# Kernel optimization log

Measured on AMD Instinct MI355X. Metric: run time of the kernel, lower is better.

## Reference

```python
import jax, jax.numpy as jnp
import numpy as np

H, C = 8, 32          # heads, channels per head; H*C = 256 triggers the LN branch
N_NODES = 30000       # nodes per node type
N_EDGES = 100000      # edges per edge type
N_TYPES = 6           # hardwired edge types (all src = Package_Name)
D_IN = 128            # raw input feature dim (Package_Name stays at 128)
LRELU_SLOPE = 0.2     # PyG GATConv default negative_slope


def _segment_softmax(e, dst, n):
    # softmax of per-edge logits e [E,H] grouped by destination node
    m = jax.ops.segment_max(e, dst, num_segments=n)
    ex = jnp.exp(e - m[dst])
    den = jax.ops.segment_sum(ex, dst, num_segments=n)
    return ex / (den[dst] + 1e-16)


def _gat(x_src, x_tgt, src, dst, Ws, Wd, a_s, a_d, b):
    # bipartite GATConv, concat heads, no self loops, no edge features
    hs = (x_src @ Ws).reshape(-1, H, C)   # [Ns,H,C]
    hd = (x_tgt @ Wd).reshape(-1, H, C)   # [Nt,H,C]
    es = jnp.einsum('nhc,hc->nh', hs, a_s)
    ed = jnp.einsum('nhc,hc->nh', hd, a_d)
    e = jax.nn.leaky_relu(es[src] + ed[dst], negative_slope=LRELU_SLOPE)  # [E,H]
    n = x_tgt.shape[0]
    alpha = _segment_softmax(e, dst, n)                                   # [E,H]
    msg = hs[src] * alpha[:, :, None]                                     # [E,H,C]
    out = jax.ops.segment_sum(msg, dst, num_segments=n).reshape(n, H * C) + b
    return out, alpha


def _ln_relu(x, g, b):
    mu = x.mean(-1, keepdims=True)
    var = ((x - mu) ** 2).mean(-1, keepdims=True)
    return jax.nn.relu((x - mu) / jnp.sqrt(var + 1e-5) * g + b)


def setup_inputs() -> dict:
    key = jax.random.key(0)
    ks = jax.random.split(key, 16)
    s = 0.05
    return {
        'x_pkg': jax.random.normal(ks[0], (N_NODES, D_IN), jnp.float32),
        'x_tgt': jax.random.normal(ks[1], (N_TYPES, N_NODES, D_IN), jnp.float32),
        'edge_index': jax.random.randint(ks[2], (N_TYPES, 2, N_EDGES), 0, N_NODES, jnp.int32),
        'W1_src': jax.random.normal(ks[3], (N_TYPES, D_IN, H * C), jnp.float32) * s,
        'W1_dst': jax.random.normal(ks[4], (N_TYPES, D_IN, H * C), jnp.float32) * s,
        'att1_src': jax.random.normal(ks[5], (N_TYPES, H, C), jnp.float32) * s,
        'att1_dst': jax.random.normal(ks[6], (N_TYPES, H, C), jnp.float32) * s,
        'b1': jnp.zeros((N_TYPES, H * C), jnp.float32),
        'W2_src': jax.random.normal(ks[7], (N_TYPES, D_IN, H * C), jnp.float32) * s,
        'W2_dst': jax.random.normal(ks[8], (N_TYPES, H * C, H * C), jnp.float32) * s,
        'att2_src': jax.random.normal(ks[9], (N_TYPES, H, C), jnp.float32) * s,
        'att2_dst': jax.random.normal(ks[10], (N_TYPES, H, C), jnp.float32) * s,
        'b2': jnp.zeros((N_TYPES, H * C), jnp.float32),
        'gamma': jnp.ones((N_TYPES, H * C), jnp.float32),
        'beta': jnp.zeros((N_TYPES, H * C), jnp.float32),
        'Wc': jax.random.normal(ks[11], (N_TYPES * H * C + D_IN, 1), jnp.float32) * s,
        'bc': jnp.zeros((1,), jnp.float32),
    }


def reference(x_pkg, x_tgt, edge_index, W1_src, W1_dst, att1_src, att1_dst, b1,
              W2_src, W2_dst, att2_src, att2_dst, b2, gamma, beta, Wc, bc):
    def layer(xt, ei, Ws, Wd, a_s, a_d, bb):
        return _gat(x_pkg, xt, ei[0], ei[1], Ws, Wd, a_s, a_d, bb)

    vlayer = jax.vmap(layer, in_axes=(0, 0, 0, 0, 0, 0, 0))

    # layer 1: Package_Name -> each of 6 target types; Package_Name itself unchanged
    out1, _ = vlayer(x_tgt, edge_index, W1_src, W1_dst, att1_src, att1_dst, b1)
    x1 = jax.vmap(_ln_relu)(out1, gamma, beta)   # module reuses ln1 after both layers

    # layer 2: src features are still the raw 128-d Package_Name features
    out2, alpha2 = vlayer(x1, edge_index, W2_src, W2_dst, att2_src, att2_dst, b2)
    x2 = jax.vmap(_ln_relu)(out2, gamma, beta)

    # global mean pool per node type, concat (6 targets then Package_Name), classify
    pooled = jnp.concatenate([x2.mean(axis=1).reshape(-1), x_pkg.mean(axis=0)])
    logits = pooled @ Wc[:, 0] + bc[0]
    return logits, alpha2
```

## Files before the change

kernel.cpp:

```cpp
#include <hip/hip_runtime.h>
#include <hip/hip_bf16.h>
#include <cstddef>

#define N_NODES 30000
#define N_EDGES 100000
#define N_TYPES 6
#define D_IN 128
#define HC 256
#define NH 8
#define CH 32

typedef __attribute__((ext_vector_type(8))) unsigned short ushort8_t;
typedef __attribute__((ext_vector_type(4))) unsigned short ushort4_t;
typedef __attribute__((ext_vector_type(8))) __bf16 bf16x8;
typedef __attribute__((ext_vector_type(4))) float floatx4;

#define L2_NPB 16
#define L2_GRID ((N_NODES + L2_NPB - 1) / L2_NPB)

__device__ inline unsigned short f2bf(float f) {
    unsigned u = __float_as_uint(f);
    u += 0x7fffu + ((u >> 16) & 1u);
    return (unsigned short)(u >> 16);
}
__device__ inline float bf2f(unsigned short u) {
    return __uint_as_float(((unsigned)u) << 16);
}

__global__ void zero4(float4* __restrict__ p, int n4) {
    int g = blockIdx.x * blockDim.x + threadIdx.x;
    if (g < n4) p[g] = make_float4(0.f, 0.f, 0.f, 0.f);
}
__global__ void zero_i(int* __restrict__ p, int n) {
    int g = blockIdx.x * blockDim.x + threadIdx.x;
    if (g < n) p[g] = 0;
}
__global__ void to_bf16(const float* __restrict__ x, unsigned short* __restrict__ o, int n4) {
    int g = blockIdx.x * blockDim.x + threadIdx.x;
    if (g >= n4) return;
    float4 v = ((const float4*)x)[g];
    ushort4_t p;
    p[0] = f2bf(v.x); p[1] = f2bf(v.y); p[2] = f2bf(v.z); p[3] = f2bf(v.w);
    *(ushort4_t*)&o[(size_t)g * 4] = p;
}

__global__ void hist_all(const int* __restrict__ ei, int* __restrict__ counts) {
    int t = blockIdx.y;
    int e = blockIdx.x * 256 + threadIdx.x;
    if (e < N_EDGES)
        atomicAdd(&counts[t * N_NODES + ei[(size_t)t * 2 * N_EDGES + N_EDGES + e]], 1);
}

#define SCAN_T 1024
#define SCAN_C 30
__global__ __launch_bounds__(1024) void scan_all(const int* __restrict__ counts_g,
                                                 int* __restrict__ row_ptr_g,
                                                 int* __restrict__ cursor_g) {
    int t = blockIdx.x;
    const int* counts = counts_g + t * N_NODES;
    int* row_ptr = row_ptr_g + t * (N_NODES + 1);
    int* cursor = cursor_g + t * N_NODES;
    __shared__ int part[SCAN_T];
    int tid = threadIdx.x;
    int base = tid * SCAN_C;
    int loc[SCAN_C];
    int s = 0;
    #pragma unroll
    for (int i = 0; i < SCAN_C; ++i) {
        int idx = base + i;
        int v = (idx < N_NODES) ? counts[idx] : 0;
        loc[i] = s; s += v;
    }
    part[tid] = s;
    __syncthreads();
    int tot = s;
    for (int d = 1; d < SCAN_T; d <<= 1) {
        int v = (tid >= d) ? part[tid - d] : 0;
        __syncthreads();
        part[tid] += v;
        __syncthreads();
    }
    int off = part[tid] - tot;
    #pragma unroll
    for (int i = 0; i < SCAN_C; ++i) {
        int idx = base + i;
        if (idx < N_NODES) { int r = off + loc[i]; row_ptr[idx] = r; cursor[idx] = r; }
    }
    if (tid == SCAN_T - 1) row_ptr[N_NODES] = part[SCAN_T - 1];
}

__global__ void fill_all(const int* __restrict__ ei, int* __restrict__ cursor,
                         int* __restrict__ elist) {
    int t = blockIdx.y;
    int e = blockIdx.x * 256 + threadIdx.x;
    if (e < N_EDGES) {
        const int* src = ei + (size_t)t * 2 * N_EDGES;
        const int* dst = src + N_EDGES;
        int pos = atomicAdd(&cursor[t * N_NODES + dst[e]], 1);
        elist[t * N_EDGES + pos] = src[e];
    }
}

__global__ void att_weight_all(const float* __restrict__ W1d, const float* __restrict__ a1d,
                               const float* __restrict__ W2d, const float* __restrict__ a2d,
                               float* __restrict__ wd1, float* __restrict__ wd2) {
    int g = blockIdx.x * blockDim.x + threadIdx.x;
    const int per_t = (D_IN + HC) * NH;
    if (g >= N_TYPES * per_t) return;
    int t = g / per_t, r = g % per_t;
    if (r < D_IN * NH) {
        int k = r >> 3, h = r & 7;
        const float* wr = W1d + (size_t)t * D_IN * HC + (size_t)k * HC + h * CH;
        const float* ar = a1d + t * HC + h * CH;
        float s = 0.f;
        #pragma unroll
        for (int c = 0; c < CH; ++c) s += wr[c] * ar[c];
        wd1[t * D_IN * NH + h * D_IN + k] = s;
    } else {
        r -= D_IN * NH;
        int k = r >> 3, h = r & 7;
        const float* wr = W2d + (size_t)t * HC * HC + (size_t)k * HC + h * CH;
        const float* ar = a2d + t * HC + h * CH;
        float s = 0.f;
        #pragma unroll
        for (int c = 0; c < CH; ++c) s += wr[c] * ar[c];
        wd2[t * HC * NH + h * HC + k] = s;
    }
}

__global__ __launch_bounds__(256) void ed1_all(const float* __restrict__ x_tgt,
                                               const float* __restrict__ wd1,
                                               float* __restrict__ ed1g) {
    const int t = blockIdx.y;
    const int lane = threadIdx.x & 63;
    const int wv = threadIdx.x >> 6;
    const int n8 = lane >> 3, h = lane & 7;
    const int node = blockIdx.x * 32 + wv * 8 + n8;
    if (node >= N_NODES) return;
    const float* xr = x_tgt + ((size_t)t * N_NODES + node) * D_IN;
    const float* wp = wd1 + t * D_IN * NH + h * D_IN;
    float acc = 0.f;
    #pragma unroll
    for (int k = 0; k < D_IN; k += 4) {
        const float4 x4 = *(const float4*)&xr[k];
        const float4 w4 = *(const float4*)&wp[k];
        acc += x4.x * w4.x + x4.y * w4.y + x4.z * w4.z + x4.w * w4.w;
    }
    ed1g[((size_t)t * N_NODES + node) * NH + h] = acc;
}

__global__ __launch_bounds__(256) void gemm_all(const unsigned short* __restrict__ A,
                                                const float* __restrict__ W1s,
                                                const float* __restrict__ W2s,
                                                const float* __restrict__ att1,
                                                const float* __restrict__ att2,
                                                unsigned short* __restrict__ hs_all,
                                                float* __restrict__ es_all) {
    const int j = blockIdx.z;
    const float* B = (j < 6) ? W1s + (size_t)j * D_IN * HC
                             : W2s + (size_t)(j - 6) * D_IN * HC;
    const float* att = (j < 6) ? att1 + j * HC : att2 + (j - 6) * HC;
    unsigned short* Cp = hs_all + (size_t)j * N_NODES * HC;
    float* e_out = es_all + (size_t)j * N_NODES * NH;

    __shared__ unsigned short As[64 * 40];
    __shared__ unsigned short Bs[64 * 40];

    const int tid = threadIdx.x;
    const int w = tid >> 6;
    const int lane = tid & 63;
    const int col = lane & 15;
    const int quad = lane >> 4;
    const int m0 = blockIdx.x * 64;
    const int n0 = blockIdx.y * 64;

    const int am = tid >> 2;
    const int ak = (tid & 3) * 8;
    const int bk2 = (tid >> 4) * 2;
    const int bn4 = (tid & 15) * 4;

    floatx4 acc[4];
    #pragma unroll
    for (int ct = 0; ct < 4; ++ct) acc[ct] = (floatx4){0.f, 0.f, 0.f, 0.f};

    #pragma unroll
    for (int k0 = 0; k0 < D_IN; k0 += 32) {
        {
            int gm = m0 + am;
            ushort8_t v = (ushort8_t){0, 0, 0, 0, 0, 0, 0, 0};
            if (gm < N_NODES) v = *(const ushort8_t*)&A[(size_t)gm * D_IN + k0 + ak];
            *(ushort8_t*)&As[am * 40 + ak] = v;
        }
        {
            const float4 r0 = *(const float4*)&B[(size_t)(k0 + bk2) * HC + n0 + bn4];
            const float4 r1 = *(const float4*)&B[(size_t)(k0 + bk2 + 1) * HC + n0 + bn4];
            float a0[4] = {r0.x, r0.y, r0.z, r0.w};
            float a1[4] = {r1.x, r1.y, r1.z, r1.w};
            #pragma unroll
            for (int q = 0; q < 4; ++q) {
                unsigned pk = (unsigned)f2bf(a0[q]) | ((unsigned)f2bf(a1[q]) << 16);
                *(unsigned*)&Bs[(bn4 + q) * 40 + bk2] = pk;
            }
        }
        __syncthreads();
        {
            ushort8_t araw = *(const ushort8_t*)&As[(w * 16 + col) * 40 + quad * 8];
            bf16x8 af = __builtin_bit_cast(bf16x8, araw);
            #pragma unroll
            for (int ct = 0; ct < 4; ++ct) {
                ushort8_t braw = *(const ushort8_t*)&Bs[(ct * 16 + col) * 40 + quad * 8];
                bf16x8 bf = __builtin_bit_cast(bf16x8, braw);
                acc[ct] = __builtin_amdgcn_mfma_f32_16x16x32_bf16(af, bf, acc[ct], 0, 0, 0);
            }
        }
        __syncthreads();
    }

    #pragma unroll
    for (int ct = 0; ct < 4; ++ct) {
        #pragma unroll
        for (int r = 0; r < 4; ++r) {
            int gm = m0 + w * 16 + quad * 4 + r;
            if (gm < N_NODES) Cp[(size_t)gm * HC + n0 + ct * 16 + col] = f2bf(acc[ct][r]);
        }
    }

    float attv[4];
    #pragma unroll
    for (int ct = 0; ct < 4; ++ct) attv[ct] = att[n0 + ct * 16 + col];
    const int hbase = n0 >> 5;
    #pragma unroll
    for (int r = 0; r < 4; ++r) {
        float h0v = acc[0][r] * attv[0] + acc[1][r] * attv[1];
        float h1v = acc[2][r] * attv[2] + acc[3][r] * attv[3];
        #pragma unroll
        for (int off = 1; off < 16; off <<= 1) {
            h0v += __shfl_xor(h0v, off);
            h1v += __shfl_xor(h1v, off);
        }
        if (col == 0) {
            int gm = m0 + w * 16 + quad * 4 + r;
            if (gm < N_NODES) {
                e_out[gm * NH + hbase] = h0v;
                e_out[gm * NH + hbase + 1] = h1v;
            }
        }
    }
}

__device__ inline void edge4(const float* __restrict__ es,
                             const unsigned short* __restrict__ hs,
                             int s_pre, int i, int cm,
                             int h_l, int lane, float ed_mine,
                             float& den, float4& acc) {
    const int i1 = (i + 1 < cm) ? i + 1 : cm;
    const int i2 = (i + 2 < cm) ? i + 2 : cm;
    const int i3 = (i + 3 < cm) ? i + 3 : cm;
    const int s0 = __shfl(s_pre, i);
    const int s1 = __shfl(s_pre, i1);
    const int s2 = __shfl(s_pre, i2);
    const int s3 = __shfl(s_pre, i3);
    float q0 = es[s0 * NH + h_l];
    float q1 = es[s1 * NH + h_l];
    float q2 = es[s2 * NH + h_l];
    float q3 = es[s3 * NH + h_l];
    const ushort4_t v0 = *(const ushort4_t*)&hs[(size_t)s0 * HC + lane * 4];
    const ushort4_t v1 = *(const ushort4_t*)&hs[(size_t)s1 * HC + lane * 4];
    const ushort4_t v2 = *(const ushort4_t*)&hs[(size_t)s2 * HC + lane * 4];
    const ushort4_t v3 = *(const ushort4_t*)&hs[(size_t)s3 * HC + lane * 4];
    q0 += ed_mine; q0 = (q0 >= 0.f) ? q0 : 0.2f * q0;
    q1 += ed_mine; q1 = (q1 >= 0.f) ? q1 : 0.2f * q1;
    q2 += ed_mine; q2 = (q2 >= 0.f) ? q2 : 0.2f * q2;
    q3 += ed_mine; q3 = (q3 >= 0.f) ? q3 : 0.2f * q3;
    const float x0 = __expf(q0);
    const float x1 = (i + 1 <= cm) ? __expf(q1) : 0.f;
    const float x2 = (i + 2 <= cm) ? __expf(q2) : 0.f;
    const float x3 = (i + 3 <= cm) ? __expf(q3) : 0.f;
    den += (x0 + x1) + (x2 + x3);
    acc.x += x0 * bf2f(v0[0]) + x1 * bf2f(v1[0]) + x2 * bf2f(v2[0]) + x3 * bf2f(v3[0]);
    acc.y += x0 * bf2f(v0[1]) + x1 * bf2f(v1[1]) + x2 * bf2f(v2[1]) + x3 * bf2f(v3[1]);
    acc.z += x0 * bf2f(v0[2]) + x1 * bf2f(v1[2]) + x2 * bf2f(v2[2]) + x3 * bf2f(v3[2]);
    acc.w += x0 * bf2f(v0[3]) + x1 * bf2f(v1[3]) + x2 * bf2f(v2[3]) + x3 * bf2f(v3[3]);
}

__device__ inline void edge1(const float* __restrict__ es,
                             const unsigned short* __restrict__ hs,
                             int s, int h_l, int lane, float ed_mine,
                             float& den, float4& acc) {
    float x = es[s * NH + h_l] + ed_mine;
    x = (x >= 0.f) ? x : 0.2f * x;
    const float ex = __expf(x);
    den += ex;
    const ushort4_t hv = *(const ushort4_t*)&hs[(size_t)s * HC + lane * 4];
    acc.x += ex * bf2f(hv[0]); acc.y += ex * bf2f(hv[1]);
    acc.z += ex * bf2f(hv[2]); acc.w += ex * bf2f(hv[3]);
}

__global__ __launch_bounds__(256) void gather_l1_all(const int* __restrict__ row_ptr_g,
                                                     const int* __restrict__ elist_g,
                                                     const float* __restrict__ es_all,
                                                     const float* __restrict__ ed1g,
                                                     const unsigned short* __restrict__ hs_all,
                                                     const float* __restrict__ b1,
                                                     const float* __restrict__ gamma,
                                                     const float* __restrict__ beta,
                                                     const float* __restrict__ wd2,
                                                     float* __restrict__ ed2g_all) {
    const int t = blockIdx.y;
    const int* row_ptr = row_ptr_g + t * (N_NODES + 1);
    const int* elist = elist_g + t * N_EDGES;
    const float* es = es_all + (size_t)t * N_NODES * NH;
    const unsigned short* hs = hs_all + (size_t)t * N_NODES * HC;
    const float* bias = b1 + t * HC;
    const float* gam = gamma + t * HC;
    const float* bet = beta + t * HC;
    const float* w2 = wd2 + t * HC * NH;
    float* ed2g = ed2g_all + (size_t)t * N_NODES * NH;

    const int lane = threadIdx.x & 63;
    const int w = threadIdx.x >> 6;
    const int d = blockIdx.x * 4 + w;
    const int h_l = lane >> 3;

    const float ed_mine = ed1g[((size_t)t * N_NODES + d) * NH + h_l];
    const int e0 = row_ptr[d], e1n = row_ptr[d + 1];
    const int cnt = e1n - e0;
    int s_pre = 0;
    if (lane < cnt) s_pre = elist[e0 + lane];

    float den = 0.f;
    float4 acc = make_float4(0.f, 0.f, 0.f, 0.f);
    if (cnt > 0) {
        const int c1 = (cnt < 64) ? cnt : 64;
        const int cm = c1 - 1;
        for (int i = 0; i < c1; i += 4)
            edge4(es, hs, s_pre, i, cm, h_l, lane, ed_mine, den, acc);
        if (cnt > 64)
            for (int ii = e0 + 64; ii < e1n; ++ii)
                edge1(es, hs, elist[ii], h_l, lane, ed_mine, den, acc);
    }

    const float inv = 1.f / (den + 1e-16f);
    const float4 bv = *(const float4*)&bias[lane * 4];
    acc.x = acc.x * inv + bv.x; acc.y = acc.y * inv + bv.y;
    acc.z = acc.z * inv + bv.z; acc.w = acc.w * inv + bv.w;

    float s1 = acc.x + acc.y + acc.z + acc.w;
    float s2 = acc.x * acc.x + acc.y * acc.y + acc.z * acc.z + acc.w * acc.w;
    #pragma unroll
    for (int off = 1; off < 64; off <<= 1) { s1 += __shfl_xor(s1, off); s2 += __shfl_xor(s2, off); }
    const float mu = s1 * (1.f / 256.f);
    const float var = s2 * (1.f / 256.f) - mu * mu;
    const float rstd = rsqrtf(var + 1e-5f);
    const float4 g4 = *(const float4*)&gam[lane * 4];
    const float4 b4 = *(const float4*)&bet[lane * 4];
    const float ya0 = fmaxf((acc.x - mu) * rstd * g4.x + b4.x, 0.f);
    const float ya1 = fmaxf((acc.y - mu) * rstd * g4.y + b4.y, 0.f);
    const float ya2 = fmaxf((acc.z - mu) * rstd * g4.z + b4.z, 0.f);
    const float ya3 = fmaxf((acc.w - mu) * rstd * g4.w + b4.w, 0.f);

    __shared__ __align__(16) float ya_s[4][256];
    {
        const int c0 = lane * 4;
        const int widx = (c0 & ~31) | ((c0 & 31) ^ ((lane >> 3) << 2));
        *(float4*)&ya_s[w][widx] = make_float4(ya0, ya1, ya2, ya3);
    }
    const int k8 = lane >> 3;
    const int h = lane & 7;
    const float* w2h = w2 + h * HC;
    float e2 = 0.f;
    #pragma unroll
    for (int jj = 0; jj < 8; ++jj) {
        const int idx = k8 * 32 + ((jj * 4) ^ (k8 << 2));
        const float4 y = *(const float4*)&ya_s[w][idx];
        const float4 wv = *(const float4*)&w2h[k8 * 32 + jj * 4];
        e2 += y.x * wv.x + y.y * wv.y + y.z * wv.z + y.w * wv.w;
    }
    e2 += __shfl_xor(e2, 8);
    e2 += __shfl_xor(e2, 16);
    e2 += __shfl_xor(e2, 32);
    if (lane < 8) ed2g[d * NH + lane] = e2;
}

__global__ __launch_bounds__(256) void gather_l2_all(const int* __restrict__ row_ptr_g,
                                                     const int* __restrict__ elist_g,
                                                     const float* __restrict__ es_all,
                                                     const float* __restrict__ ed2g_all,
                                                     const unsigned short* __restrict__ hs_all,
                                                     const float* __restrict__ b2,
                                                     const float* __restrict__ gamma,
                                                     const float* __restrict__ beta,
                                                     float* __restrict__ deng_all,
                                                     float* __restrict__ ppart) {
    const int t = blockIdx.y;
    const int* row_ptr = row_ptr_g + t * (N_NODES + 1);
    const int* elist = elist_g + t * N_EDGES;
    const float* es = es_all + (size_t)(6 + t) * N_NODES * NH;
    const float* ed2g = ed2g_all + (size_t)t * N_NODES * NH;
    const unsigned short* hs = hs_all + (size_t)(6 + t) * N_NODES * HC;
    const float* bias = b2 + t * HC;
    const float* gam = gamma + t * HC;
    const float* bet = beta + t * HC;
    float* deng = deng_all + (size_t)t * N_NODES * NH;
    float* psum_part = ppart + (size_t)t * L2_GRID * HC;

    const int tid = threadIdx.x;
    const int lane = tid & 63;
    const int w = tid >> 6;
    const int h_l = lane >> 3;
    const float4 bv = *(const float4*)&bias[lane * 4];
    const float4 g4 = *(const float4*)&gam[lane * 4];
    const float4 b4 = *(const float4*)&bet[lane * 4];

    float4 pool = make_float4(0.f, 0.f, 0.f, 0.f);
    const int base = blockIdx.x * L2_NPB;

    #pragma unroll 1
    for (int rep = 0; rep < L2_NPB / 4; ++rep) {
        const int d = base + rep * 4 + w;
        if (d >= N_NODES) break;

        const float ed_mine = ed2g[d * NH + h_l];
        const int e0 = row_ptr[d], e1n = row_ptr[d + 1];
        const int cnt = e1n - e0;
        int s_pre = 0;
        if (lane < cnt) s_pre = elist[e0 + lane];

        float den = 0.f;
        float4 acc = make_float4(0.f, 0.f, 0.f, 0.f);
        if (cnt > 0) {
            const int c1 = (cnt < 64) ? cnt : 64;
            const int cm = c1 - 1;
            for (int i = 0; i < c1; i += 4)
                edge4(es, hs, s_pre, i, cm, h_l, lane, ed_mine, den, acc);
            if (cnt > 64)
                for (int ii = e0 + 64; ii < e1n; ++ii)
                    edge1(es, hs, elist[ii], h_l, lane, ed_mine, den, acc);
        }
        if ((lane & 7) == 0) deng[d * NH + h_l] = den;
        const float inv = 1.f / (den + 1e-16f);
        acc.x = acc.x * inv + bv.x; acc.y = acc.y * inv + bv.y;
        acc.z = acc.z * inv + bv.z; acc.w = acc.w * inv + bv.w;

        float s1 = acc.x + acc.y + acc.z + acc.w;
        float s2 = acc.x * acc.x + acc.y * acc.y + acc.z * acc.z + acc.w * acc.w;
        #pragma unroll
        for (int off = 1; off < 64; off <<= 1) { s1 += __shfl_xor(s1, off); s2 += __shfl_xor(s2, off); }
        const float mu = s1 * (1.f / 256.f);
        const float var = s2 * (1.f / 256.f) - mu * mu;
        const float rstd = rsqrtf(var + 1e-5f);
        pool.x += fmaxf((acc.x - mu) * rstd * g4.x + b4.x, 0.f);
        pool.y += fmaxf((acc.y - mu) * rstd * g4.y + b4.y, 0.f);
        pool.z += fmaxf((acc.z - mu) * rstd * g4.z + b4.z, 0.f);
        pool.w += fmaxf((acc.w - mu) * rstd * g4.w + b4.w, 0.f);
    }

    __shared__ __align__(16) float sacc[4][260];
    *(float4*)&sacc[w][lane * 4] = pool;
    __syncthreads();
    float tot = sacc[0][tid] + sacc[1][tid] + sacc[2][tid] + sacc[3][tid];
    psum_part[(size_t)blockIdx.x * HC + tid] = tot;
}

__global__ __launch_bounds__(256) void pool_reduce_all(const float* __restrict__ ppart,
                                                       float* __restrict__ psums) {
    int t = blockIdx.y;
    const float* part = ppart + (size_t)t * L2_GRID * HC;
    int tid = threadIdx.x;
    float acc = 0.f;
    for (int b = blockIdx.x; b < L2_GRID; b += gridDim.x)
        acc += part[(size_t)b * HC + tid];
    atomicAdd(&psums[t * HC + tid], acc);
}

__global__ void alpha_all(const int* __restrict__ ei,
                          const float* __restrict__ es_all,
                          const float* __restrict__ ed2g_all,
                          const float* __restrict__ deng_all,
                          float* __restrict__ out) {
    int t = blockIdx.y;
    int g = blockIdx.x * 256 + threadIdx.x;
    if (g >= N_EDGES * NH) return;
    int e = g >> 3, h = g & 7;
    const int* src = ei + (size_t)t * 2 * N_EDGES;
    const int* dst = src + N_EDGES;
    int s = src[e], d = dst[e];
    const float* es = es_all + (size_t)(6 + t) * N_NODES * NH;
    float x = es[s * NH + h] + ed2g_all[(size_t)t * N_NODES * NH + d * NH + h];
    x = (x >= 0.f) ? x : 0.2f * x;
    out[(size_t)t * N_EDGES * NH + g] =
        __expf(x) / (deng_all[(size_t)t * N_NODES * NH + d * NH + h] + 1e-16f);
}

__global__ __launch_bounds__(256) void pkg_accum(const float* __restrict__ x, float* __restrict__ sums) {
    int tid = threadIdx.x;
    int col = tid & 127;
    int rof = tid >> 7;
    float acc = 0.f;
    for (int r = blockIdx.x * 2 + rof; r < N_NODES; r += gridDim.x * 2)
        acc += x[(size_t)r * D_IN + col];
    atomicAdd(&sums[col], acc);
}

__global__ __launch_bounds__(256) void logits_k(const float* __restrict__ psums,
                                                const float* __restrict__ ksums,
                                                const float* __restrict__ Wc,
                                                const float* __restrict__ bc,
                                                float* __restrict__ out) {
    int tid = threadIdx.x;
    const float inv = 1.f / (float)N_NODES;
    float acc = 0.f;
    for (int i = tid; i < N_TYPES * HC; i += 256) acc += psums[i] * inv * Wc[i];
    if (tid < D_IN) acc += ksums[tid] * inv * Wc[N_TYPES * HC + tid];
    #pragma unroll
    for (int off = 32; off; off >>= 1) acc += __shfl_down(acc, off);
    __shared__ float w[4];
    if ((tid & 63) == 0) w[tid >> 6] = acc;
    __syncthreads();
    if (tid == 0) out[0] = w[0] + w[1] + w[2] + w[3] + bc[0];
}

static inline void zf(float* p, int n, hipStream_t stream) {
    int n4 = (n + 3) >> 2;
    zero4<<<(n4 + 255) / 256, 256, 0, stream>>>((float4*)p, n4);
}

extern "C" void kernel_launch(void* const* d_in, const int* in_sizes, int n_in,
                              void* d_out, int out_size, void* d_ws, size_t ws_size,
                              hipStream_t stream) {
    const float* x_pkg    = (const float*)d_in[0];
    const float* x_tgt    = (const float*)d_in[1];
    const int*   ei       = (const int*)d_in[2];
    const float* W1_src   = (const float*)d_in[3];
    const float* W1_dst   = (const float*)d_in[4];
    const float* att1_src = (const float*)d_in[5];
    const float* att1_dst = (const float*)d_in[6];
    const float* b1       = (const float*)d_in[7];
    const float* W2_src   = (const float*)d_in[8];
    const float* W2_dst   = (const float*)d_in[9];
    const float* att2_src = (const float*)d_in[10];
    const float* att2_dst = (const float*)d_in[11];
    const float* b2       = (const float*)d_in[12];
    const float* gamma    = (const float*)d_in[13];
    const float* beta     = (const float*)d_in[14];
    const float* Wc       = (const float*)d_in[15];
    const float* bc       = (const float*)d_in[16];
    float* out = (float*)d_out;

    char* wsb = (char*)d_ws;
    unsigned short* xpkg_bf = (unsigned short*)wsb;
    unsigned short* hs_all  = xpkg_bf + (size_t)N_NODES * D_IN;
    float* es_all   = (float*)(hs_all + (size_t)12 * N_NODES * HC);
    float* ed2g_all = es_all + (size_t)12 * N_NODES * NH;
    float* deng_all = ed2g_all + (size_t)N_TYPES * N_NODES * NH;
    float* psums    = deng_all + (size_t)N_TYPES * N_NODES * NH;
    float* ksums    = psums + N_TYPES * HC;
    float* wd1      = ksums + D_IN;
    float* wd2      = wd1 + N_TYPES * D_IN * NH;
    float* ed1g     = wd2 + N_TYPES * HC * NH;
    float* ppart    = ed1g + (size_t)N_TYPES * N_NODES * NH;
    int* counts  = (int*)(ppart + (size_t)N_TYPES * L2_GRID * HC);
    int* row_ptr = counts + N_TYPES * N_NODES;
    int* cursor  = row_ptr + N_TYPES * (N_NODES + 1);
    int* elist   = cursor + N_TYPES * N_NODES;

    dim3 egrid((N_EDGES + 255) / 256, N_TYPES);

    zf(psums, N_TYPES * HC, stream);
    zf(ksums, D_IN, stream);
    pkg_accum<<<256, 256, 0, stream>>>(x_pkg, ksums);
    {
        int tot = N_TYPES * (D_IN + HC) * NH;
        att_weight_all<<<(tot + 255) / 256, 256, 0, stream>>>(W1_dst, att1_dst, W2_dst, att2_dst, wd1, wd2);
    }
    {
        dim3 g((N_NODES + 31) / 32, N_TYPES);
        ed1_all<<<g, 256, 0, stream>>>(x_tgt, wd1, ed1g);
    }
    to_bf16<<<((N_NODES * D_IN / 4) + 255) / 256, 256, 0, stream>>>(x_pkg, xpkg_bf, N_NODES * D_IN / 4);
    zero_i<<<(N_TYPES * N_NODES + 255) / 256, 256, 0, stream>>>(counts, N_TYPES * N_NODES);
    hist_all<<<egrid, 256, 0, stream>>>(ei, counts);
    scan_all<<<N_TYPES, SCAN_T, 0, stream>>>(counts, row_ptr, cursor);
    fill_all<<<egrid, 256, 0, stream>>>(ei, cursor, elist);

    {
        dim3 g((N_NODES + 63) / 64, HC / 64, 12);
        gemm_all<<<g, 256, 0, stream>>>(xpkg_bf, W1_src, W2_src, att1_src, att2_src,
                                        hs_all, es_all);
    }

    {
        dim3 g(N_NODES / 4, N_TYPES);
        gather_l1_all<<<g, 256, 0, stream>>>(row_ptr, elist, es_all, ed1g, hs_all,
                                             b1, gamma, beta, wd2, ed2g_all);
    }

    {
        dim3 g(L2_GRID, N_TYPES);
        gather_l2_all<<<g, 256, 0, stream>>>(row_ptr, elist, es_all, ed2g_all, hs_all,
                                             b2, gamma, beta, deng_all, ppart);
    }
    {
        dim3 g(8, N_TYPES);
        pool_reduce_all<<<g, 256, 0, stream>>>(ppart, psums);
    }
    {
        dim3 g((N_EDGES * NH + 255) / 256, N_TYPES);
        alpha_all<<<g, 256, 0, stream>>>(ei, es_all, ed2g_all, deng_all, out + 1);
    }

    logits_k<<<1, 256, 0, stream>>>(psums, ksums, Wc, bc, out);
}
```

Measured before the change: 880.2 us.

## Fuse layer-1 and layer-2 gathers into one kernel with small-degree fast path

Layer 1 and layer 2 attention gathers now run in one kernel per destination node. The layer-2 logit term is kept in registers through a shuffle instead of being reloaded from global memory, and the second launch is removed. For nodes with at most four edges, the neighbour rows and logits for both layers are loaded together up front to hide latency. The trade-offs are a larger per-block pool partial buffer (one row per 4 nodes instead of per 16), more reduction work in pool_reduce (grid widened), and higher register pressure.

```diff
diff --git a/kernel.cpp b/kernel.cpp
--- a/kernel.cpp
+++ b/kernel.cpp
@@ -15,8 +15,7 @@
 typedef __attribute__((ext_vector_type(8))) __bf16 bf16x8;
 typedef __attribute__((ext_vector_type(4))) float floatx4;
 
-#define L2_NPB 16
-#define L2_GRID ((N_NODES + L2_NPB - 1) / L2_NPB)
+#define FG_GRID (N_NODES / 4)
 
 __device__ inline unsigned short f2bf(float f) {
     unsigned u = __float_as_uint(f);
@@ -296,26 +295,27 @@
     acc.z += ex * bf2f(hv[2]); acc.w += ex * bf2f(hv[3]);
 }
 
-__global__ __launch_bounds__(256) void gather_l1_all(const int* __restrict__ row_ptr_g,
-                                                     const int* __restrict__ elist_g,
-                                                     const float* __restrict__ es_all,
-                                                     const float* __restrict__ ed1g,
-                                                     const unsigned short* __restrict__ hs_all,
-                                                     const float* __restrict__ b1,
-                                                     const float* __restrict__ gamma,
-                                                     const float* __restrict__ beta,
-                                                     const float* __restrict__ wd2,
-                                                     float* __restrict__ ed2g_all) {
+__global__ __launch_bounds__(256) void fused_gather_all(
+        const int* __restrict__ row_ptr_g, const int* __restrict__ elist_g,
+        const float* __restrict__ es_all, const float* __restrict__ ed1g,
+        const unsigned short* __restrict__ hs_all,
+        const float* __restrict__ b1, const float* __restrict__ b2,
+        const float* __restrict__ gamma, const float* __restrict__ beta,
+        const float* __restrict__ wd2,
+        float* __restrict__ ed2g_all, float* __restrict__ deng_all,
+        float* __restrict__ ppart) {
     const int t = blockIdx.y;
     const int* row_ptr = row_ptr_g + t * (N_NODES + 1);
     const int* elist = elist_g + t * N_EDGES;
-    const float* es = es_all + (size_t)t * N_NODES * NH;
-    const unsigned short* hs = hs_all + (size_t)t * N_NODES * HC;
-    const float* bias = b1 + t * HC;
+    const float* es1 = es_all + (size_t)t * N_NODES * NH;
+    const float* es2 = es_all + (size_t)(6 + t) * N_NODES * NH;
+    const unsigned short* hs1 = hs_all + (size_t)t * N_NODES * HC;
+    const unsigned short* hs2 = hs_all + (size_t)(6 + t) * N_NODES * HC;
     const float* gam = gamma + t * HC;
     const float* bet = beta + t * HC;
     const float* w2 = wd2 + t * HC * NH;
     float* ed2g = ed2g_all + (size_t)t * N_NODES * NH;
+    float* deng = deng_all + (size_t)t * N_NODES * NH;
 
     const int lane = threadIdx.x & 63;
     const int w = threadIdx.x >> 6;
@@ -328,25 +328,66 @@
     int s_pre = 0;
     if (lane < cnt) s_pre = elist[e0 + lane];
 
-    float den = 0.f;
-    float4 acc = make_float4(0.f, 0.f, 0.f, 0.f);
-    if (cnt > 0) {
+    float den1 = 0.f, den2 = 0.f;
+    float4 acc1 = make_float4(0.f, 0.f, 0.f, 0.f);
+    float4 acc2 = make_float4(0.f, 0.f, 0.f, 0.f);
+
+    float q20, q21, q22, q23;
+    ushort4_t v20, v21, v22, v23;
+    const bool fast = (cnt > 0) && (cnt <= 4);
+
+    if (fast) {
+        const int cm = cnt - 1;
+        const int s0 = __shfl(s_pre, 0);
+        const int s1 = __shfl(s_pre, (1 < cm) ? 1 : cm);
+        const int s2 = __shfl(s_pre, (2 < cm) ? 2 : cm);
+        const int s3 = __shfl(s_pre, cm);
+        float q10 = es1[s0 * NH + h_l];
+        float q11 = es1[s1 * NH + h_l];
+        float q12 = es1[s2 * NH + h_l];
+        float q13 = es1[s3 * NH + h_l];
+        const ushort4_t v10 = *(const ushort4_t*)&hs1[(size_t)s0 * HC + lane * 4];
+        const ushort4_t v11 = *(const ushort4_t*)&hs1[(size_t)s1 * HC + lane * 4];
+        const ushort4_t v12 = *(const ushort4_t*)&hs1[(size_t)s2 * HC + lane * 4];
+        const ushort4_t v13 = *(const ushort4_t*)&hs1[(size_t)s3 * HC + lane * 4];
+        q20 = es2[s0 * NH + h_l];
+        q21 = es2[s1 * NH + h_l];
+        q22 = es2[s2 * NH + h_l];
+        q23 = es2[s3 * NH + h_l];
+        v20 = *(const ushort4_t*)&hs2[(size_t)s0 * HC + lane * 4];
+        v21 = *(const ushort4_t*)&hs2[(size_t)s1 * HC + lane * 4];
+        v22 = *(const ushort4_t*)&hs2[(size_t)s2 * HC + lane * 4];
+        v23 = *(const ushort4_t*)&hs2[(size_t)s3 * HC + lane * 4];
+        q10 += ed_mine; q10 = (q10 >= 0.f) ? q10 : 0.2f * q10;
+        q11 += ed_mine; q11 = (q11 >= 0.f) ? q11 : 0.2f * q11;
+        q12 += ed_mine; q12 = (q12 >= 0.f) ? q12 : 0.2f * q12;
+        q13 += ed_mine; q13 = (q13 >= 0.f) ? q13 : 0.2f * q13;
+        const float x0 = __expf(q10);
+        const float x1 = (cnt > 1) ? __expf(q11) : 0.f;
+        const float x2 = (cnt > 2) ? __expf(q12) : 0.f;
+        const float x3 = (cnt > 3) ? __expf(q13) : 0.f;
+        den1 = (x0 + x1) + (x2 + x3);
+        acc1.x = x0 * bf2f(v10[0]) + x1 * bf2f(v11[0]) + x2 * bf2f(v12[0]) + x3 * bf2f(v13[0]);
+        acc1.y = x0 * bf2f(v10[1]) + x1 * bf2f(v11[1]) + x2 * bf2f(v12[1]) + x3 * bf2f(v13[1]);
+        acc1.z = x0 * bf2f(v10[2]) + x1 * bf2f(v11[2]) + x2 * bf2f(v12[2]) + x3 * bf2f(v13[2]);
+        acc1.w = x0 * bf2f(v10[3]) + x1 * bf2f(v11[3]) + x2 * bf2f(v12[3]) + x3 * bf2f(v13[3]);
+    } else if (cnt > 0) {
         const int c1 = (cnt < 64) ? cnt : 64;
         const int cm = c1 - 1;
         for (int i = 0; i < c1; i += 4)
-            edge4(es, hs, s_pre, i, cm, h_l, lane, ed_mine, den, acc);
+            edge4(es1, hs1, s_pre, i, cm, h_l, lane, ed_mine, den1, acc1);
         if (cnt > 64)
             for (int ii = e0 + 64; ii < e1n; ++ii)
-                edge1(es, hs, elist[ii], h_l, lane, ed_mine, den, acc);
-    }
-
-    const float inv = 1.f / (den + 1e-16f);
-    const float4 bv = *(const float4*)&bias[lane * 4];
-    acc.x = acc.x * inv + bv.x; acc.y = acc.y * inv + bv.y;
-    acc.z = acc.z * inv + bv.z; acc.w = acc.w * inv + bv.w;
-
-    float s1 = acc.x + acc.y + acc.z + acc.w;
-    float s2 = acc.x * acc.x + acc.y * acc.y + acc.z * acc.z + acc.w * acc.w;
+                edge1(es1, hs1, elist[ii], h_l, lane, ed_mine, den1, acc1);
+    }
+
+    const float inv1 = 1.f / (den1 + 1e-16f);
+    const float4 bv1 = *(const float4*)&b1[t * HC + lane * 4];
+    acc1.x = acc1.x * inv1 + bv1.x; acc1.y = acc1.y * inv1 + bv1.y;
+    acc1.z = acc1.z * inv1 + bv1.z; acc1.w = acc1.w * inv1 + bv1.w;
+
+    float s1 = acc1.x + acc1.y + acc1.z + acc1.w;
+    float s2 = acc1.x * acc1.x + acc1.y * acc1.y + acc1.z * acc1.z + acc1.w * acc1.w;
     #pragma unroll
     for (int off = 1; off < 64; off <<= 1) { s1 += __shfl_xor(s1, off); s2 += __shfl_xor(s2, off); }
     const float mu = s1 * (1.f / 256.f);
@@ -354,10 +395,10 @@
     const float rstd = rsqrtf(var + 1e-5f);
     const float4 g4 = *(const float4*)&gam[lane * 4];
     const float4 b4 = *(const float4*)&bet[lane * 4];
-    const float ya0 = fmaxf((acc.x - mu) * rstd * g4.x + b4.x, 0.f);
-    const float ya1 = fmaxf((acc.y - mu) * rstd * g4.y + b4.y, 0.f);
-    const float ya2 = fmaxf((acc.z - mu) * rstd * g4.z + b4.z, 0.f);
-    const float ya3 = fmaxf((acc.w - mu) * rstd * g4.w + b4.w, 0.f);
+    const float ya0 = fmaxf((acc1.x - mu) * rstd * g4.x + b4.x, 0.f);
+    const float ya1 = fmaxf((acc1.y - mu) * rstd * g4.y + b4.y, 0.f);
+    const float ya2 = fmaxf((acc1.z - mu) * rstd * g4.z + b4.z, 0.f);
+    const float ya3 = fmaxf((acc1.w - mu) * rstd * g4.w + b4.w, 0.f);
 
     __shared__ __align__(16) float ya_s[4][256];
     {
@@ -366,8 +407,8 @@
         *(float4*)&ya_s[w][widx] = make_float4(ya0, ya1, ya2, ya3);
     }
     const int k8 = lane >> 3;
-    const int h = lane & 7;
-    const float* w2h = w2 + h * HC;
+    const int hh = lane & 7;
+    const float* w2h = w2 + hh * HC;
     float e2 = 0.f;
     #pragma unroll
     for (int jj = 0; jj < 8; ++jj) {
@@ -380,95 +421,66 @@
     e2 += __shfl_xor(e2, 16);
     e2 += __shfl_xor(e2, 32);
     if (lane < 8) ed2g[d * NH + lane] = e2;
-}
-
-__global__ __launch_bounds__(256) void gather_l2_all(const int* __restrict__ row_ptr_g,
-                                                     const int* __restrict__ elist_g,
-                                                     const float* __restrict__ es_all,
-                                                     const float* __restrict__ ed2g_all,
-                                                     const unsigned short* __restrict__ hs_all,
-                                                     const float* __restrict__ b2,
-                                                     const float* __restrict__ gamma,
-                                                     const float* __restrict__ beta,
-                                                     float* __restrict__ deng_all,
-                                                     float* __restrict__ ppart) {
-    const int t = blockIdx.y;
-    const int* row_ptr = row_ptr_g + t * (N_NODES + 1);
-    const int* elist = elist_g + t * N_EDGES;
-    const float* es = es_all + (size_t)(6 + t) * N_NODES * NH;
-    const float* ed2g = ed2g_all + (size_t)t * N_NODES * NH;
-    const unsigned short* hs = hs_all + (size_t)(6 + t) * N_NODES * HC;
-    const float* bias = b2 + t * HC;
-    const float* gam = gamma + t * HC;
-    const float* bet = beta + t * HC;
-    float* deng = deng_all + (size_t)t * N_NODES * NH;
-    float* psum_part = ppart + (size_t)t * L2_GRID * HC;
-
-    const int tid = threadIdx.x;
-    const int lane = tid & 63;
-    const int w = tid >> 6;
-    const int h_l = lane >> 3;
-    const float4 bv = *(const float4*)&bias[lane * 4];
-    const float4 g4 = *(const float4*)&gam[lane * 4];
-    const float4 b4 = *(const float4*)&bet[lane * 4];
-
-    float4 pool = make_float4(0.f, 0.f, 0.f, 0.f);
-    const int base = blockIdx.x * L2_NPB;
-
-    #pragma unroll 1
-    for (int rep = 0; rep < L2_NPB / 4; ++rep) {
-        const int d = base + rep * 4 + w;
-        if (d >= N_NODES) break;
-
-        const float ed_mine = ed2g[d * NH + h_l];
-        const int e0 = row_ptr[d], e1n = row_ptr[d + 1];
-        const int cnt = e1n - e0;
-        int s_pre = 0;
-        if (lane < cnt) s_pre = elist[e0 + lane];
-
-        float den = 0.f;
-        float4 acc = make_float4(0.f, 0.f, 0.f, 0.f);
-        if (cnt > 0) {
-            const int c1 = (cnt < 64) ? cnt : 64;
-            const int cm = c1 - 1;
-            for (int i = 0; i < c1; i += 4)
-                edge4(es, hs, s_pre, i, cm, h_l, lane, ed_mine, den, acc);
-            if (cnt > 64)
-                for (int ii = e0 + 64; ii < e1n; ++ii)
-                    edge1(es, hs, elist[ii], h_l, lane, ed_mine, den, acc);
-        }
-        if ((lane & 7) == 0) deng[d * NH + h_l] = den;
-        const float inv = 1.f / (den + 1e-16f);
-        acc.x = acc.x * inv + bv.x; acc.y = acc.y * inv + bv.y;
-        acc.z = acc.z * inv + bv.z; acc.w = acc.w * inv + bv.w;
-
-        float s1 = acc.x + acc.y + acc.z + acc.w;
-        float s2 = acc.x * acc.x + acc.y * acc.y + acc.z * acc.z + acc.w * acc.w;
-        #pragma unroll
-        for (int off = 1; off < 64; off <<= 1) { s1 += __shfl_xor(s1, off); s2 += __shfl_xor(s2, off); }
-        const float mu = s1 * (1.f / 256.f);
-        const float var = s2 * (1.f / 256.f) - mu * mu;
-        const float rstd = rsqrtf(var + 1e-5f);
-        pool.x += fmaxf((acc.x - mu) * rstd * g4.x + b4.x, 0.f);
-        pool.y += fmaxf((acc.y - mu) * rstd * g4.y + b4.y, 0.f);
-        pool.z += fmaxf((acc.z - mu) * rstd * g4.z + b4.z, 0.f);
-        pool.w += fmaxf((acc.w - mu) * rstd * g4.w + b4.w, 0.f);
-    }
+    const float ed2_mine = __shfl(e2, h_l);
+
+    if (fast) {
+        q20 += ed2_mine; q20 = (q20 >= 0.f) ? q20 : 0.2f * q20;
+        q21 += ed2_mine; q21 = (q21 >= 0.f) ? q21 : 0.2f * q21;
+        q22 += ed2_mine; q22 = (q22 >= 0.f) ? q22 : 0.2f * q22;
+        q23 += ed2_mine; q23 = (q23 >= 0.f) ? q23 : 0.2f * q23;
+        const float x0 = __expf(q20);
+        const float x1 = (cnt > 1) ? __expf(q21) : 0.f;
+        const float x2 = (cnt > 2) ? __expf(q22) : 0.f;
+        const float x3 = (cnt > 3) ? __expf(q23) : 0.f;
+        den2 = (x0 + x1) + (x2 + x3);
+        acc2.x = x0 * bf2f(v20[0]) + x1 * bf2f(v21[0]) + x2 * bf2f(v22[0]) + x3 * bf2f(v23[0]);
+        acc2.y = x0 * bf2f(v20[1]) + x1 * bf2f(v21[1]) + x2 * bf2f(v22[1]) + x3 * bf2f(v23[1]);
+        acc2.z = x0 * bf2f(v20[2]) + x1 * bf2f(v21[2]) + x2 * bf2f(v22[2]) + x3 * bf2f(v23[2]);
+        acc2.w = x0 * bf2f(v20[3]) + x1 * bf2f(v21[3]) + x2 * bf2f(v22[3]) + x3 * bf2f(v23[3]);
+    } else if (cnt > 0) {
+        const int c1 = (cnt < 64) ? cnt : 64;
+        const int cm = c1 - 1;
+        for (int i = 0; i < c1; i += 4)
+            edge4(es2, hs2, s_pre, i, cm, h_l, lane, ed2_mine, den2, acc2);
+        if (cnt > 64)
+            for (int ii = e0 + 64; ii < e1n; ++ii)
+                edge1(es2, hs2, elist[ii], h_l, lane, ed2_mine, den2, acc2);
+    }
+
+    if ((lane & 7) == 0) deng[d * NH + h_l] = den2;
+    const float inv2 = 1.f / (den2 + 1e-16f);
+    const float4 bv2 = *(const float4*)&b2[t * HC + lane * 4];
+    acc2.x = acc2.x * inv2 + bv2.x; acc2.y = acc2.y * inv2 + bv2.y;
+    acc2.z = acc2.z * inv2 + bv2.z; acc2.w = acc2.w * inv2 + bv2.w;
+
+    float t1 = acc2.x + acc2.y + acc2.z + acc2.w;
+    float t2 = acc2.x * acc2.x + acc2.y * acc2.y + acc2.z * acc2.z + acc2.w * acc2.w;
+    #pragma unroll
+    for (int off = 1; off < 64; off <<= 1) { t1 += __shfl_xor(t1, off); t2 += __shfl_xor(t2, off); }
+    const float mu2 = t1 * (1.f / 256.f);
+    const float var2 = t2 * (1.f / 256.f) - mu2 * mu2;
+    const float rstd2 = rsqrtf(var2 + 1e-5f);
+    float4 pool;
+    pool.x = fmaxf((acc2.x - mu2) * rstd2 * g4.x + b4.x, 0.f);
+    pool.y = fmaxf((acc2.y - mu2) * rstd2 * g4.y + b4.y, 0.f);
+    pool.z = fmaxf((acc2.z - mu2) * rstd2 * g4.z + b4.z, 0.f);
+    pool.w = fmaxf((acc2.w - mu2) * rstd2 * g4.w + b4.w, 0.f);
 
     __shared__ __align__(16) float sacc[4][260];
     *(float4*)&sacc[w][lane * 4] = pool;
     __syncthreads();
+    const int tid = threadIdx.x;
     float tot = sacc[0][tid] + sacc[1][tid] + sacc[2][tid] + sacc[3][tid];
-    psum_part[(size_t)blockIdx.x * HC + tid] = tot;
+    ppart[((size_t)t * FG_GRID + blockIdx.x) * HC + tid] = tot;
 }
 
 __global__ __launch_bounds__(256) void pool_reduce_all(const float* __restrict__ ppart,
                                                        float* __restrict__ psums) {
     int t = blockIdx.y;
-    const float* part = ppart + (size_t)t * L2_GRID * HC;
+    const float* part = ppart + (size_t)t * FG_GRID * HC;
     int tid = threadIdx.x;
     float acc = 0.f;
-    for (int b = blockIdx.x; b < L2_GRID; b += gridDim.x)
+    for (int b = blockIdx.x; b < FG_GRID; b += gridDim.x)
         acc += part[(size_t)b * HC + tid];
     atomicAdd(&psums[t * HC + tid], acc);
 }
@@ -559,7 +571,7 @@
     float* wd2      = wd1 + N_TYPES * D_IN * NH;
     float* ed1g     = wd2 + N_TYPES * HC * NH;
     float* ppart    = ed1g + (size_t)N_TYPES * N_NODES * NH;
-    int* counts  = (int*)(ppart + (size_t)N_TYPES * L2_GRID * HC);
+    int* counts  = (int*)(ppart + (size_t)N_TYPES * FG_GRID * HC);
     int* row_ptr = counts + N_TYPES * N_NODES;
     int* cursor  = row_ptr + N_TYPES * (N_NODES + 1);
     int* elist   = cursor + N_TYPES * N_NODES;
@@ -590,18 +602,13 @@
     }
 
     {
-        dim3 g(N_NODES / 4, N_TYPES);
-        gather_l1_all<<<g, 256, 0, stream>>>(row_ptr, elist, es_all, ed1g, hs_all,
-                                             b1, gamma, beta, wd2, ed2g_all);
-    }
-
+        dim3 g(FG_GRID, N_TYPES);
+        fused_gather_all<<<g, 256, 0, stream>>>(row_ptr, elist, es_all, ed1g, hs_all,
+                                                b1, b2, gamma, beta, wd2,
+                                                ed2g_all, deng_all, ppart);
+    }
     {
-        dim3 g(L2_GRID, N_TYPES);
-        gather_l2_all<<<g, 256, 0, stream>>>(row_ptr, elist, es_all, ed2g_all, hs_all,
-                                             b2, gamma, beta, deng_all, ppart);
-    }
-    {
-        dim3 g(8, N_TYPES);
+        dim3 g(32, N_TYPES);
         pool_reduce_all<<<g, 256, 0, stream>>>(ppart, psums);
     }
     {
```

Measured after the change: 885.2 us. Within noise of the previous version (+0.6%).
